# Optimization experiments

Measured on AMD Instinct MI355X. Metric: run time of the kernel, lower is better.

Reference implementation:

```python
import jax, jax.numpy as jnp
import numpy as np

N_NODES = 100000
N_EDGES = 600000
NUM_GRAPHS = 512
IN_DIM = 128
HID = 64
HEADS = 2
NEG_SLOPE = 0.2


def gat_layer(h_in, src, dst, W, a_s, a_d, b, n_nodes):
    # W: [F_in, H*C], a_s/a_d: [H, C], b: [H*C]
    H, C = a_s.shape
    h = (h_in @ W).reshape(n_nodes, H, C)            # [N,H,C]
    alpha_src = jnp.einsum('nhc,hc->nh', h, a_s)      # [N,H]
    alpha_dst = jnp.einsum('nhc,hc->nh', h, a_d)      # [N,H]
    e = alpha_src[src] + alpha_dst[dst]               # [E,H]
    e = jnp.where(e >= 0, e, NEG_SLOPE * e)           # leaky_relu
    # segment softmax over destination node
    m = jax.ops.segment_max(e, dst, num_segments=n_nodes)
    m = jnp.where(jnp.isfinite(m), m, 0.0)
    ex = jnp.exp(e - m[dst])                          # [E,H]
    denom = jax.ops.segment_sum(ex, dst, num_segments=n_nodes)
    alpha = ex / jnp.maximum(denom[dst], 1e-16)       # [E,H]
    out = jax.ops.segment_sum(alpha[:, :, None] * h[src], dst, num_segments=n_nodes)
    return out.reshape(n_nodes, H * C) + b


def setup_inputs() -> dict:
    key = jax.random.key(0)
    ks = jax.random.split(key, 16)
    x = jax.random.normal(ks[0], (N_NODES, IN_DIM), dtype=jnp.float32)
    edge_index = jax.random.randint(ks[1], (2, N_EDGES), 0, N_NODES, dtype=jnp.int32)
    batch = jnp.sort(jax.random.randint(ks[2], (N_NODES,), 0, NUM_GRAPHS, dtype=jnp.int32))
    s = lambda *d: 1.0 / np.sqrt(d[0])
    W1 = jax.random.normal(ks[3], (IN_DIM, HEADS * HID), jnp.float32) * s(IN_DIM)
    a_src1 = jax.random.normal(ks[4], (HEADS, HID), jnp.float32) * s(HID)
    a_dst1 = jax.random.normal(ks[5], (HEADS, HID), jnp.float32) * s(HID)
    b1 = jnp.zeros((HEADS * HID,), jnp.float32)
    W2 = jax.random.normal(ks[6], (HEADS * HID, HID), jnp.float32) * s(HEADS * HID)
    a_src2 = jax.random.normal(ks[7], (1, HID), jnp.float32) * s(HID)
    a_dst2 = jax.random.normal(ks[8], (1, HID), jnp.float32) * s(HID)
    b2 = jnp.zeros((HID,), jnp.float32)
    Wf1 = jax.random.normal(ks[9], (2 * HID, HID), jnp.float32) * s(2 * HID)
    bf1 = jnp.zeros((HID,), jnp.float32)
    Wf2 = jax.random.normal(ks[10], (HID, 1), jnp.float32) * s(HID)
    bf2 = jnp.zeros((1,), jnp.float32)
    return dict(x=x, edge_index=edge_index, batch=batch, W1=W1, a_src1=a_src1,
                a_dst1=a_dst1, b1=b1, W2=W2, a_src2=a_src2, a_dst2=a_dst2, b2=b2,
                Wf1=Wf1, bf1=bf1, Wf2=Wf2, bf2=bf2)


def reference(x, edge_index, batch, W1, a_src1, a_dst1, b1, W2, a_src2, a_dst2, b2,
              Wf1, bf1, Wf2, bf2):
    n = x.shape[0]
    loops = jnp.arange(n, dtype=edge_index.dtype)
    src = jnp.concatenate([edge_index[0], loops])
    dst = jnp.concatenate([edge_index[1], loops])
    h = gat_layer(x, src, dst, W1, a_src1, a_dst1, b1, n)
    h = jax.nn.relu(h)
    h = gat_layer(h, src, dst, W2, a_src2, a_dst2, b2, n)  # [N, HID]
    # global mean + max pool per graph
    ones = jnp.ones((n,), h.dtype)
    counts = jax.ops.segment_sum(ones, batch, num_segments=NUM_GRAPHS)  # [G]
    mean = jax.ops.segment_sum(h, batch, num_segments=NUM_GRAPHS) / jnp.maximum(counts, 1.0)[:, None]
    mx = jax.ops.segment_max(h, batch, num_segments=NUM_GRAPHS)
    mx = jnp.where(counts[:, None] > 0, mx, 0.0)
    pooled = jnp.concatenate([mean, mx], axis=1)  # [G, 2*HID]
    out = jax.nn.relu(pooled @ Wf1 + bf1) @ Wf2 + bf2  # [G, 1]
    return out
```

## Files before the change

kernel.cpp:

```cpp
#include <hip/hip_runtime.h>

#define N_NODESC 100000
#define N_EDGESC 600000
#define E_TOTC   700000
#define NUM_GRAPHSC 512
#define NEG_SLOPE 0.2f
#define NEG_INF_ENC 0x007FFFFFu
#define SCAN_NB 128

typedef unsigned short ushort_t;
typedef __attribute__((ext_vector_type(8))) short bf16x8;
typedef __attribute__((ext_vector_type(4))) float f32x4;

__device__ __forceinline__ unsigned enc_f32(float f) {
    unsigned u = __float_as_uint(f);
    return (u & 0x80000000u) ? ~u : (u | 0x80000000u);
}
__device__ __forceinline__ float dec_f32(unsigned u) {
    u = (u & 0x80000000u) ? (u ^ 0x80000000u) : ~u;
    return __uint_as_float(u);
}
__device__ __forceinline__ ushort_t f32_to_bf16(float f) {
    unsigned u = __float_as_uint(f);
    return (ushort_t)((u + 0x7FFFu + ((u >> 16) & 1u)) >> 16);
}
__device__ __forceinline__ float bf16_to_f32(ushort_t h) {
    return __uint_as_float(((unsigned)h) << 16);
}
__device__ __forceinline__ unsigned pack_bf16x2(float a, float b) {
    return (unsigned)f32_to_bf16(a) | ((unsigned)f32_to_bf16(b) << 16);
}

__global__ __launch_bounds__(256) void init_all(float* __restrict__ msum,
                                                unsigned* __restrict__ mmax,
                                                float* __restrict__ cnt,
                                                int* __restrict__ deg,
                                                const float* __restrict__ W1,
                                                const float* __restrict__ W2,
                                                ushort_t* __restrict__ wPre1,
                                                ushort_t* __restrict__ wPre2,
                                                float* __restrict__ alphas) {
    int i = blockIdx.x * 256 + threadIdx.x;
    if (i < NUM_GRAPHSC * 64) { msum[i] = 0.f; mmax[i] = NEG_INF_ENC; }
    if (i < NUM_GRAPHSC) cnt[i] = 0.f;
    if (i < N_NODESC) deg[i] = 0;
    if (i < 6 * N_NODESC) alphas[i] = 0.f;
    if (i < 128 * 128) {
        int n = i >> 7, k = i & 127;
        wPre1[n * 128 + k] = f32_to_bf16(W1[k * 128 + n]);
    } else if (i < 128 * 128 + 64 * 128) {
        int j = i - 128 * 128;
        int n = j >> 7, k = j & 127;
        wPre2[n * 128 + k] = f32_to_bf16(W2[k * 64 + n]);
    }
}

__global__ __launch_bounds__(256) void hist_dst(const int* __restrict__ ei,
                                                int* __restrict__ deg) {
    int e = blockIdx.x * blockDim.x + threadIdx.x;
    if (e >= E_TOTC) return;
    int d = (e < N_EDGESC) ? ei[N_EDGESC + e] : e - N_EDGESC;
    atomicAdd(&deg[d], 1);
}

__global__ __launch_bounds__(256) void scan_partial(const int* __restrict__ deg,
                                                    int* __restrict__ bsum, int n) {
    __shared__ int red[256];
    int chunk = (n + SCAN_NB - 1) / SCAN_NB;
    int lo = blockIdx.x * chunk, hi = min(lo + chunk, n);
    int s = 0;
    for (int i = lo + threadIdx.x; i < hi; i += 256) s += deg[i];
    red[threadIdx.x] = s;
    __syncthreads();
    for (int d = 128; d; d >>= 1) {
        if (threadIdx.x < d) red[threadIdx.x] += red[threadIdx.x + d];
        __syncthreads();
    }
    if (threadIdx.x == 0) bsum[blockIdx.x] = red[0];
}

__global__ __launch_bounds__(256) void scan_final(const int* __restrict__ deg,
                                                  const int* __restrict__ bsum,
                                                  int* __restrict__ off, int n) {
    __shared__ int bs[SCAN_NB];
    __shared__ int tile[256];
    __shared__ int carry;
    int t = threadIdx.x;
    if (t < SCAN_NB) bs[t] = bsum[t];
    __syncthreads();
    for (int d = 1; d < SCAN_NB; d <<= 1) {
        int v = (t >= d && t < SCAN_NB) ? bs[t - d] : 0;
        __syncthreads();
        if (t < SCAN_NB) bs[t] += v;
        __syncthreads();
    }
    if (t == 0) carry = blockIdx.x ? bs[blockIdx.x - 1] : 0;
    __syncthreads();
    int chunk = (n + SCAN_NB - 1) / SCAN_NB;
    int lo = blockIdx.x * chunk, hi = min(lo + chunk, n);
    for (int base = lo; base < hi; base += 256) {
        int i = base + t;
        int v = (i < hi) ? deg[i] : 0;
        tile[t] = v;
        __syncthreads();
        for (int d = 1; d < 256; d <<= 1) {
            int u = (t >= d) ? tile[t - d] : 0;
            __syncthreads();
            tile[t] += u;
            __syncthreads();
        }
        if (i < hi) off[i] = carry + tile[t] - v;
        __syncthreads();
        if (t == 0) carry += tile[255];
        __syncthreads();
    }
}

__global__ __launch_bounds__(256) void scatter_csr(const int* __restrict__ ei,
                                                   int* __restrict__ off,
                                                   int* __restrict__ csr) {
    int e = blockIdx.x * blockDim.x + threadIdx.x;
    if (e >= E_TOTC) return;
    int s, d;
    if (e < N_EDGESC) { s = ei[e]; d = ei[N_EDGESC + e]; } else { s = d = e - N_EDGESC; }
    int slot = atomicAdd(&off[d], 1);
    csr[slot] = s;
}

__global__ __launch_bounds__(256) void gemm1_mfma(const float* __restrict__ X,
                                                  const ushort_t* __restrict__ Wp,
                                                  const float* __restrict__ a_s,
                                                  const float* __restrict__ a_d,
                                                  float* __restrict__ as_out,
                                                  float* __restrict__ ad_out,
                                                  ushort_t* __restrict__ Y16, int N) {
    int tid = threadIdx.x;
    int wave = tid >> 6, lane = tid & 63;
    int quad = lane >> 4, l16 = lane & 15;
    size_t node0 = (size_t)blockIdx.x * 16;

    size_t arow = node0 + l16;
    if (arow >= (size_t)N) arow = N - 1;
    const float* xp = X + arow * 128;
    float4 xa[4], xb[4];
#pragma unroll
    for (int kc = 0; kc < 4; ++kc) {
        xa[kc] = *(const float4*)(xp + kc * 32 + quad * 8);
        xb[kc] = *(const float4*)(xp + kc * 32 + quad * 8 + 4);
    }

    const ushort_t* bp0 = Wp + (size_t)(wave * 16 + l16) * 128;
    const ushort_t* bp1 = Wp + (size_t)((wave + 4) * 16 + l16) * 128;

    f32x4 acc0 = (f32x4){0.f, 0.f, 0.f, 0.f};
    f32x4 acc1 = (f32x4){0.f, 0.f, 0.f, 0.f};

#pragma unroll
    for (int kc = 0; kc < 4; ++kc) {
        int kb = kc * 32 + quad * 8;
        union { bf16x8 v; unsigned u[4]; } af;
        af.u[0] = pack_bf16x2(xa[kc].x, xa[kc].y);
        af.u[1] = pack_bf16x2(xa[kc].z, xa[kc].w);
        af.u[2] = pack_bf16x2(xb[kc].x, xb[kc].y);
        af.u[3] = pack_bf16x2(xb[kc].z, xb[kc].w);
        bf16x8 b0 = *(const bf16x8*)(bp0 + kb);
        bf16x8 b1 = *(const bf16x8*)(bp1 + kb);
        acc0 = __builtin_amdgcn_mfma_f32_16x16x32_bf16(af.v, b0, acc0, 0, 0, 0);
        acc1 = __builtin_amdgcn_mfma_f32_16x16x32_bf16(af.v, b1, acc1, 0, 0, 0);
    }

    unsigned* Yu = (unsigned*)Y16;
    int c = wave * 16 + l16;
    float as0v = a_s[c], as1v = a_s[64 + c];
    float ad0v = a_d[c], ad1v = a_d[64 + c];
#pragma unroll
    for (int r = 0; r < 4; ++r) {
        size_t row = node0 + quad * 4 + r;
        bool ok = row < (size_t)N;
        if (ok) Yu[row * 64 + c] = pack_bf16x2(acc0[r], acc1[r]);
        float ps = acc0[r] * as0v, pd = acc0[r] * ad0v;
        float qs = acc1[r] * as1v, qd = acc1[r] * ad1v;
#pragma unroll
        for (int sh = 1; sh < 16; sh <<= 1) {
            ps += __shfl_xor(ps, sh);
            pd += __shfl_xor(pd, sh);
            qs += __shfl_xor(qs, sh);
            qd += __shfl_xor(qd, sh);
        }
        if (l16 == 0 && ok) {
            atomicAdd(&as_out[row * 2 + 0], ps);
            atomicAdd(&ad_out[row * 2 + 0], pd);
            atomicAdd(&as_out[row * 2 + 1], qs);
            atomicAdd(&ad_out[row * 2 + 1], qd);
        }
    }
}

__global__ __launch_bounds__(256) void gemm2_mfma(const ushort_t* __restrict__ Xb,
                                                  const ushort_t* __restrict__ Wp,
                                                  const float* __restrict__ a_s,
                                                  const float* __restrict__ a_d,
                                                  float* __restrict__ as_out,
                                                  float* __restrict__ ad_out,
                                                  ushort_t* __restrict__ Y16, int N) {
    int tid = threadIdx.x;
    int wave = tid >> 6, lane = tid & 63;
    int quad = lane >> 4, l16 = lane & 15;
    size_t node0 = (size_t)blockIdx.x * 16;

    size_t arow = node0 + l16;
    if (arow >= (size_t)N) arow = N - 1;
    const ushort_t* xp = Xb + arow * 128;
    bf16x8 a[4];
#pragma unroll
    for (int kc = 0; kc < 4; ++kc)
        a[kc] = *(const bf16x8*)(xp + kc * 32 + quad * 8);

    const ushort_t* bp = Wp + (size_t)(wave * 16 + l16) * 128;
    f32x4 acc = (f32x4){0.f, 0.f, 0.f, 0.f};
#pragma unroll
    for (int kc = 0; kc < 4; ++kc) {
        int kb = kc * 32 + quad * 8;
        bf16x8 b = *(const bf16x8*)(bp + kb);
        acc = __builtin_amdgcn_mfma_f32_16x16x32_bf16(a[kc], b, acc, 0, 0, 0);
    }

    int c = wave * 16 + l16;
    float asv = a_s[c], adv = a_d[c];
#pragma unroll
    for (int r = 0; r < 4; ++r) {
        size_t row = node0 + quad * 4 + r;
        bool ok = row < (size_t)N;
        if (ok) Y16[row * 64 + c] = f32_to_bf16(acc[r]);
        float ps = acc[r] * asv, pd = acc[r] * adv;
#pragma unroll
        for (int sh = 1; sh < 16; sh <<= 1) {
            ps += __shfl_xor(ps, sh);
            pd += __shfl_xor(pd, sh);
        }
        if (l16 == 0 && ok) {
            atomicAdd(&as_out[row], ps);
            atomicAdd(&ad_out[row], pd);
        }
    }
}

template <int H, bool RELU, bool OB16>
__global__ __launch_bounds__(256) void gat_gather(const int* __restrict__ off_end,
                                                  const int* __restrict__ deg,
                                                  const int* __restrict__ csr,
                                                  const float* __restrict__ as,
                                                  const float* __restrict__ ad,
                                                  const ushort_t* __restrict__ H16,
                                                  const float* __restrict__ b,
                                                  void* __restrict__ outp, int N) {
    int lane = threadIdx.x & 63;
    int wave = threadIdx.x >> 6;
    int l = lane & 15;
    int gbase = lane & 48;
    int n = blockIdx.x * 16 + wave * 4 + (lane >> 4);
    if (n >= N) return;
    int dg = deg[n];
    int o = off_end[n] - dg;
    float adv[H];
#pragma unroll
    for (int h = 0; h < H; ++h) adv[h] = ad[n * H + h];

    float acc[H][4], den[H];
#pragma unroll
    for (int h = 0; h < H; ++h) {
        den[h] = 0.f;
#pragma unroll
        for (int q = 0; q < 4; ++q) acc[h][q] = 0.f;
    }

    const unsigned* Hu = (const unsigned*)H16;

    for (int base = 0; base < dg; base += 16) {
        int i = base + l;
        bool valid = i < dg;
        int s = valid ? csr[o + i] : 0;
        float v[H];
        if (H == 2) {
            float2 p = valid ? ((const float2*)as)[s] : make_float2(0.f, 0.f);
            v[0] = p.x + adv[0];
            v[H - 1] = p.y + adv[H - 1];
        } else {
            v[0] = valid ? as[s] + adv[0] : 0.f;
        }
#pragma unroll
        for (int h = 0; h < H; ++h) {
            float e = v[h] >= 0.f ? v[h] : NEG_SLOPE * v[h];
            v[h] = valid ? __expf(e) : 0.f;
            den[h] += v[h];
        }
        int wpk = (H == 2) ? (int)pack_bf16x2(v[0], v[H - 1])
                           : (int)__float_as_uint(v[0]);
        int cnt = min(dg - base, 16);
        int cnt4 = (cnt + 3) & ~3;
        for (int j = 0; j < cnt4; j += 4) {
#pragma unroll
            for (int u = 0; u < 4; ++u) {
                int src = gbase + j + u;
                int sj = __shfl(s, src);
                int wp = __shfl(wpk, src);
                if (H == 2) {
                    float w0 = __uint_as_float(((unsigned)wp) << 16);
                    float w1 = __uint_as_float(((unsigned)wp) & 0xffff0000u);
                    uint4 hu = *(const uint4*)(Hu + (size_t)sj * 64 + l * 4);
                    acc[0][0] += w0 * __uint_as_float(hu.x << 16);
                    acc[H - 1][0] += w1 * __uint_as_float(hu.x & 0xffff0000u);
                    acc[0][1] += w0 * __uint_as_float(hu.y << 16);
                    acc[H - 1][1] += w1 * __uint_as_float(hu.y & 0xffff0000u);
                    acc[0][2] += w0 * __uint_as_float(hu.z << 16);
                    acc[H - 1][2] += w1 * __uint_as_float(hu.z & 0xffff0000u);
                    acc[0][3] += w0 * __uint_as_float(hu.w << 16);
                    acc[H - 1][3] += w1 * __uint_as_float(hu.w & 0xffff0000u);
                } else {
                    float w0 = __uint_as_float((unsigned)wp);
                    uint2 hu = *(const uint2*)((const unsigned*)(H16 + (size_t)sj * 64) + l * 2);
                    acc[0][0] += w0 * __uint_as_float(hu.x << 16);
                    acc[0][1] += w0 * __uint_as_float(hu.x & 0xffff0000u);
                    acc[0][2] += w0 * __uint_as_float(hu.y << 16);
                    acc[0][3] += w0 * __uint_as_float(hu.y & 0xffff0000u);
                }
            }
        }
    }
#pragma unroll
    for (int h = 0; h < H; ++h) {
#pragma unroll
        for (int sh = 8; sh; sh >>= 1) den[h] += __shfl_xor(den[h], sh);
    }
    if (H == 2) {
        float4 b0 = *(const float4*)(b + l * 4);
        float4 b1 = *(const float4*)(b + 64 + l * 4);
        float r0[4], r1[4];
        float id0 = 1.f / fmaxf(den[0], 1e-16f);
        float id1 = 1.f / fmaxf(den[H - 1], 1e-16f);
        r0[0] = acc[0][0] * id0 + b0.x; r0[1] = acc[0][1] * id0 + b0.y;
        r0[2] = acc[0][2] * id0 + b0.z; r0[3] = acc[0][3] * id0 + b0.w;
        r1[0] = acc[H - 1][0] * id1 + b1.x; r1[1] = acc[H - 1][1] * id1 + b1.y;
        r1[2] = acc[H - 1][2] * id1 + b1.z; r1[3] = acc[H - 1][3] * id1 + b1.w;
        if (RELU) {
#pragma unroll
            for (int q = 0; q < 4; ++q) { r0[q] = fmaxf(r0[q], 0.f); r1[q] = fmaxf(r1[q], 0.f); }
        }
        ushort_t* outb = (ushort_t*)outp;
        uint2 p0 = make_uint2(pack_bf16x2(r0[0], r0[1]), pack_bf16x2(r0[2], r0[3]));
        uint2 p1 = make_uint2(pack_bf16x2(r1[0], r1[1]), pack_bf16x2(r1[2], r1[3]));
        *(uint2*)(outb + (size_t)n * 128 + l * 4) = p0;
        *(uint2*)(outb + (size_t)n * 128 + 64 + l * 4) = p1;
    } else {
        float4 bv = *(const float4*)(b + l * 4);
        float id0 = 1.f / fmaxf(den[0], 1e-16f);
        float4 r;
        r.x = acc[0][0] * id0 + bv.x; r.y = acc[0][1] * id0 + bv.y;
        r.z = acc[0][2] * id0 + bv.z; r.w = acc[0][3] * id0 + bv.w;
        if (RELU) { r.x = fmaxf(r.x, 0.f); r.y = fmaxf(r.y, 0.f);
                    r.z = fmaxf(r.z, 0.f); r.w = fmaxf(r.w, 0.f); }
        *(float4*)((float*)outp + (size_t)n * 64 + l * 4) = r;
    }
}

__global__ __launch_bounds__(256) void pool_nodes(const float* __restrict__ h2,
                                                  const int* __restrict__ batch,
                                                  float* __restrict__ msum,
                                                  unsigned* __restrict__ mmax,
                                                  float* __restrict__ cnt, int N) {
    int wid = threadIdx.x >> 6, lane = threadIdx.x & 63;
    int n0 = (blockIdx.x * 4 + wid) * 64;
    if (n0 >= N) return;
    int n1 = min(n0 + 64, N);
    int curg = batch[n0];
    float s = 0.f, m = -1e30f;
    int c = 0;
    for (int n = n0; n < n1; ++n) {
        int g = batch[n];
        float v = h2[(size_t)n * 64 + lane];
        if (g != curg) {
            atomicAdd(&msum[curg * 64 + lane], s);
            atomicMax(&mmax[curg * 64 + lane], enc_f32(m));
            if (lane == 0) atomicAdd(&cnt[curg], (float)c);
            s = 0.f; m = -1e30f; c = 0; curg = g;
        }
        s += v;
        m = fmaxf(m, v);
        ++c;
    }
    atomicAdd(&msum[curg * 64 + lane], s);
    atomicMax(&mmax[curg * 64 + lane], enc_f32(m));
    if (lane == 0) atomicAdd(&cnt[curg], (float)c);
}

__global__ __launch_bounds__(64) void mlp_head(const float* __restrict__ msum,
                                               const unsigned* __restrict__ mmax,
                                               const float* __restrict__ cnt,
                                               const float* __restrict__ Wf1,
                                               const float* __restrict__ bf1,
                                               const float* __restrict__ Wf2,
                                               const float* __restrict__ bf2,
                                               float* __restrict__ out) {
    __shared__ float pooled[128];
    int g = blockIdx.x, lane = threadIdx.x;
    float c = cnt[g];
    pooled[lane] = msum[g * 64 + lane] / fmaxf(c, 1.0f);
    pooled[64 + lane] = (c > 0.f) ? dec_f32(mmax[g * 64 + lane]) : 0.f;
    __syncthreads();
    float acc = bf1[lane];
#pragma unroll
    for (int k = 0; k < 128; ++k) acc += pooled[k] * Wf1[k * 64 + lane];
    acc = fmaxf(acc, 0.f);
    float r = acc * Wf2[lane];
#pragma unroll
    for (int off = 32; off; off >>= 1) r += __shfl_xor(r, off);
    if (lane == 0) out[g] = r + bf2[0];
}

extern "C" void kernel_launch(void* const* d_in, const int* in_sizes, int n_in,
                              void* d_out, int out_size, void* d_ws, size_t ws_size,
                              hipStream_t stream) {
    const float* x    = (const float*)d_in[0];
    const int*   ei   = (const int*)d_in[1];
    const int*   batch= (const int*)d_in[2];
    const float* W1   = (const float*)d_in[3];
    const float* as1  = (const float*)d_in[4];
    const float* ad1  = (const float*)d_in[5];
    const float* b1   = (const float*)d_in[6];
    const float* W2   = (const float*)d_in[7];
    const float* as2  = (const float*)d_in[8];
    const float* ad2  = (const float*)d_in[9];
    const float* b2   = (const float*)d_in[10];
    const float* Wf1  = (const float*)d_in[11];
    const float* bf1  = (const float*)d_in[12];
    const float* Wf2  = (const float*)d_in[13];
    const float* bf2  = (const float*)d_in[14];
    float* out = (float*)d_out;

    const size_t N = N_NODESC;
    float* ws = (float*)d_ws;
    ushort_t* h16_1 = (ushort_t*)ws;
    ushort_t* out1b = (ushort_t*)(ws + N * 64);
    ushort_t* h16_2 = (ushort_t*)(ws + N * 128);
    float*    out2  = ws + N * 160;
    float*    small = ws + N * 224;
    float*    as1b = small;
    float*    ad1b = small + 2 * N;
    float*    as2b = small + 4 * N;
    float*    ad2b = small + 5 * N;
    float*    msum = small + 6 * N;
    unsigned* mmax = (unsigned*)(small + 6 * N + 512 * 64);
    float*    cntb = small + 6 * N + 2 * 512 * 64;
    int* ip  = (int*)(small + 6 * N + 2 * 512 * 64 + 512);
    int* deg  = ip;
    int* off  = ip + N;
    int* csr  = ip + 2 * N;
    int* bsum = ip + 2 * N + E_TOTC;
    ushort_t* wPre1 = (ushort_t*)(bsum + SCAN_NB);
    ushort_t* wPre2 = wPre1 + 128 * 128;

    init_all<<<(6 * N_NODESC + 255) / 256, 256, 0, stream>>>(msum, mmax, cntb, deg,
                                                             W1, W2, wPre1, wPre2,
                                                             small);

    hist_dst<<<(E_TOTC + 255) / 256, 256, 0, stream>>>(ei, deg);
    scan_partial<<<SCAN_NB, 256, 0, stream>>>(deg, bsum, N);
    scan_final<<<SCAN_NB, 256, 0, stream>>>(deg, bsum, off, N);
    scatter_csr<<<(E_TOTC + 255) / 256, 256, 0, stream>>>(ei, off, csr);

    const int NBLK16G = (N_NODESC + 15) / 16;

    gemm1_mfma<<<NBLK16G, 256, 0, stream>>>(x, wPre1, as1, ad1, as1b, ad1b, h16_1, N);
    gat_gather<2, true, true><<<NBLK16G, 256, 0, stream>>>(off, deg, csr, as1b,
                                                           ad1b, h16_1, b1, out1b, N);

    gemm2_mfma<<<NBLK16G, 256, 0, stream>>>(out1b, wPre2, as2, ad2, as2b, ad2b, h16_2, N);
    gat_gather<1, false, false><<<NBLK16G, 256, 0, stream>>>(off, deg, csr, as2b,
                                                             ad2b, h16_2, b2, out2, N);

    pool_nodes<<<(N + 255) / 256, 256, 0, stream>>>(out2, batch, msum, mmax, cntb, N);
    mlp_head<<<NUM_GRAPHSC, 64, 0, stream>>>(msum, mmax, cntb, Wf1, bf1, Wf2, bf2, out);
}
```

Before: 332.1 us.

## Stage gemm1 output through LDS and retile gemm2 to 64-row blocks

gemm1 now writes its packed bf16 output into a shared-memory tile and then stores whole rows with coalesced 64-lane writes. Before, each lane wrote a scattered 4-byte word per row. A scheduling barrier separates the input loads from the MFMA loop. gemm2 is retiled so each block covers 64 nodes, with each wave computing a 32x32 tile using 2x2 MFMAs. This reuses the B fragments across two row tiles and halves the per-row attention atomics per wave, in exchange for more registers per wave and fewer blocks.

Measured after the change: 323.4 us. 2.6% less time.

```diff
diff --git a/kernel.cpp b/kernel.cpp
--- a/kernel.cpp
+++ b/kernel.cpp
@@ -134,6 +134,7 @@
                                                   float* __restrict__ as_out,
                                                   float* __restrict__ ad_out,
                                                   ushort_t* __restrict__ Y16, int N) {
+    __shared__ unsigned ytile[16][64];
     int tid = threadIdx.x;
     int wave = tid >> 6, lane = tid & 63;
     int quad = lane >> 4, l16 = lane & 15;
@@ -148,6 +149,7 @@
         xa[kc] = *(const float4*)(xp + kc * 32 + quad * 8);
         xb[kc] = *(const float4*)(xp + kc * 32 + quad * 8 + 4);
     }
+    __builtin_amdgcn_sched_barrier(0);
 
     const ushort_t* bp0 = Wp + (size_t)(wave * 16 + l16) * 128;
     const ushort_t* bp1 = Wp + (size_t)((wave + 4) * 16 + l16) * 128;
@@ -169,7 +171,6 @@
         acc1 = __builtin_amdgcn_mfma_f32_16x16x32_bf16(af.v, b1, acc1, 0, 0, 0);
     }
 
-    unsigned* Yu = (unsigned*)Y16;
     int c = wave * 16 + l16;
     float as0v = a_s[c], as1v = a_s[64 + c];
     float ad0v = a_d[c], ad1v = a_d[64 + c];
@@ -177,7 +178,7 @@
     for (int r = 0; r < 4; ++r) {
         size_t row = node0 + quad * 4 + r;
         bool ok = row < (size_t)N;
-        if (ok) Yu[row * 64 + c] = pack_bf16x2(acc0[r], acc1[r]);
+        ytile[quad * 4 + r][c] = pack_bf16x2(acc0[r], acc1[r]);
         float ps = acc0[r] * as0v, pd = acc0[r] * ad0v;
         float qs = acc1[r] * as1v, qd = acc1[r] * ad1v;
 #pragma unroll
@@ -193,6 +194,14 @@
             atomicAdd(&as_out[row * 2 + 1], qs);
             atomicAdd(&ad_out[row * 2 + 1], qd);
         }
+    }
+    __syncthreads();
+    unsigned* Yu = (unsigned*)Y16;
+#pragma unroll
+    for (int r = 0; r < 4; ++r) {
+        size_t row = node0 + wave * 4 + r;
+        if (row < (size_t)N)
+            Yu[row * 64 + lane] = ytile[wave * 4 + r][lane];
     }
 }
 
@@ -206,43 +215,65 @@
     int tid = threadIdx.x;
     int wave = tid >> 6, lane = tid & 63;
     int quad = lane >> 4, l16 = lane & 15;
-    size_t node0 = (size_t)blockIdx.x * 16;
-
-    size_t arow = node0 + l16;
-    if (arow >= (size_t)N) arow = N - 1;
-    const ushort_t* xp = Xb + arow * 128;
-    bf16x8 a[4];
-#pragma unroll
-    for (int kc = 0; kc < 4; ++kc)
-        a[kc] = *(const bf16x8*)(xp + kc * 32 + quad * 8);
-
-    const ushort_t* bp = Wp + (size_t)(wave * 16 + l16) * 128;
-    f32x4 acc = (f32x4){0.f, 0.f, 0.f, 0.f};
+    int rbase = (wave >> 1) * 32, cbase = (wave & 1) * 32;
+    size_t node0 = (size_t)blockIdx.x * 64;
+
+    bf16x8 a[2][4];
+#pragma unroll
+    for (int rt = 0; rt < 2; ++rt) {
+        size_t row = node0 + rbase + rt * 16 + l16;
+        if (row >= (size_t)N) row = N - 1;
+#pragma unroll
+        for (int kc = 0; kc < 4; ++kc)
+            a[rt][kc] = *(const bf16x8*)(Xb + row * 128 + kc * 32 + quad * 8);
+    }
+    __builtin_amdgcn_sched_barrier(0);
+
+    const ushort_t* b0p = Wp + (size_t)(cbase + l16) * 128;
+    const ushort_t* b1p = Wp + (size_t)(cbase + 16 + l16) * 128;
+
+    f32x4 acc[2][2];
+#pragma unroll
+    for (int rt = 0; rt < 2; ++rt)
+#pragma unroll
+        for (int ct = 0; ct < 2; ++ct) acc[rt][ct] = (f32x4){0.f, 0.f, 0.f, 0.f};
+
 #pragma unroll
     for (int kc = 0; kc < 4; ++kc) {
         int kb = kc * 32 + quad * 8;
-        bf16x8 b = *(const bf16x8*)(bp + kb);
-        acc = __builtin_amdgcn_mfma_f32_16x16x32_bf16(a[kc], b, acc, 0, 0, 0);
-    }
-
-    int c = wave * 16 + l16;
-    float asv = a_s[c], adv = a_d[c];
-#pragma unroll
-    for (int r = 0; r < 4; ++r) {
-        size_t row = node0 + quad * 4 + r;
-        bool ok = row < (size_t)N;
-        if (ok) Y16[row * 64 + c] = f32_to_bf16(acc[r]);
-        float ps = acc[r] * asv, pd = acc[r] * adv;
-#pragma unroll
-        for (int sh = 1; sh < 16; sh <<= 1) {
-            ps += __shfl_xor(ps, sh);
-            pd += __shfl_xor(pd, sh);
-        }
-        if (l16 == 0 && ok) {
-            atomicAdd(&as_out[row], ps);
-            atomicAdd(&ad_out[row], pd);
-        }
-    }
+        bf16x8 b0 = *(const bf16x8*)(b0p + kb);
+        bf16x8 b1 = *(const bf16x8*)(b1p + kb);
+#pragma unroll
+        for (int rt = 0; rt < 2; ++rt) {
+            acc[rt][0] = __builtin_amdgcn_mfma_f32_16x16x32_bf16(a[rt][kc], b0, acc[rt][0], 0, 0, 0);
+            acc[rt][1] = __builtin_amdgcn_mfma_f32_16x16x32_bf16(a[rt][kc], b1, acc[rt][1], 0, 0, 0);
+        }
+    }
+
+    float asv0 = a_s[cbase + l16], asv1 = a_s[cbase + 16 + l16];
+    float adv0 = a_d[cbase + l16], adv1 = a_d[cbase + 16 + l16];
+#pragma unroll
+    for (int rt = 0; rt < 2; ++rt)
+#pragma unroll
+        for (int r = 0; r < 4; ++r) {
+            size_t row = node0 + rbase + rt * 16 + quad * 4 + r;
+            bool ok = row < (size_t)N;
+            if (ok) {
+                Y16[row * 64 + cbase + l16]      = f32_to_bf16(acc[rt][0][r]);
+                Y16[row * 64 + cbase + 16 + l16] = f32_to_bf16(acc[rt][1][r]);
+            }
+            float ps = acc[rt][0][r] * asv0 + acc[rt][1][r] * asv1;
+            float pd = acc[rt][0][r] * adv0 + acc[rt][1][r] * adv1;
+#pragma unroll
+            for (int sh = 1; sh < 16; sh <<= 1) {
+                ps += __shfl_xor(ps, sh);
+                pd += __shfl_xor(pd, sh);
+            }
+            if (l16 == 0 && ok) {
+                atomicAdd(&as_out[row], ps);
+                atomicAdd(&ad_out[row], pd);
+            }
+        }
 }
 
 template <int H, bool RELU, bool OB16>
@@ -469,12 +500,13 @@
     scatter_csr<<<(E_TOTC + 255) / 256, 256, 0, stream>>>(ei, off, csr);
 
     const int NBLK16G = (N_NODESC + 15) / 16;
+    const int NBLK64  = (N_NODESC + 63) / 64;
 
     gemm1_mfma<<<NBLK16G, 256, 0, stream>>>(x, wPre1, as1, ad1, as1b, ad1b, h16_1, N);
     gat_gather<2, true, true><<<NBLK16G, 256, 0, stream>>>(off, deg, csr, as1b,
                                                            ad1b, h16_1, b1, out1b, N);
 
-    gemm2_mfma<<<NBLK16G, 256, 0, stream>>>(out1b, wPre2, as2, ad2, as2b, ad2b, h16_2, N);
+    gemm2_mfma<<<NBLK64, 256, 0, stream>>>(out1b, wPre2, as2, ad2, as2b, ad2b, h16_2, N);
     gat_gather<1, false, false><<<NBLK16G, 256, 0, stream>>>(off, deg, csr, as2b,
                                                              ad2b, h16_2, b2, out2, N);
 
```
